# Performance work log

Measured on AMD Instinct MI355X. Metric: run time of the kernel, lower is better.

The kernel has to match this reference:

```python
import jax, jax.numpy as jnp
import numpy as np

N, E, D, G, NTYPES = 50000, 400000, 64, 512, 64


def _bn(x, g, b):
    # BatchNorm1d in training mode: biased batch stats, eps=1e-5, affine g/b
    mu = x.mean(0)
    var = ((x - mu) ** 2).mean(0)
    return g * (x - mu) * jax.lax.rsqrt(var + 1e-5) + b


def _rotmat(a):
    t, p, q = a[0], a[1], a[2]
    ct, st = jnp.cos(t), jnp.sin(t)
    cp, sp = jnp.cos(p), jnp.sin(p)
    cq, sq = jnp.cos(q), jnp.sin(q)
    z = jnp.zeros(())
    o = jnp.ones(())
    Rt = jnp.array([[ct, -st, z], [st, ct, z], [z, z, o]])
    Rp = jnp.array([[cp, z, -sp], [z, o, z], [sp, z, cp]])
    Rq = jnp.array([[o, z, z], [z, cq, -sq], [z, sq, cq]])
    return Rt @ Rp @ Rq


def _egat(src, dst, nf, ef, Wnode, bnode, Wni, Wnj, Wfij, attn, H):
    # DGL EGATConv: edge feats from src/dst node + edge projections, edge-softmax attention over dst
    n = nf.shape[0]
    f_out = jax.nn.leaky_relu((nf @ Wni)[src] + (nf @ Wnj)[dst] + ef @ Wfij)  # [E, H*D]
    f_out = f_out.reshape(-1, H, D)
    e = (f_out * attn[None]).sum(-1)  # [E, H]
    emax = jax.ops.segment_max(e, dst, num_segments=n)
    ee = jnp.exp(e - emax[dst])
    a = ee / jax.ops.segment_sum(ee, dst, num_segments=n)[dst]
    hsrc = (nf @ Wnode + bnode).reshape(n, H, D)[src]
    h_out = jax.ops.segment_sum(hsrc * a[:, :, None], dst, num_segments=n)  # [N, H, D]
    return h_out, f_out


def _layer(src, dst, nh, eh, p, H, last):
    Wnode, bnode, Wni, Wnj, Wfij, attn, bnn_g, bnn_b, bne_g, bne_b, Wpn, bpn, Wpe, bpe = p
    hn, he = _egat(src, dst, nh, eh, Wnode, bnode, Wni, Wnj, Wfij, attn, H)
    if last:
        hn, he = hn.mean(1), he.mean(1)
    else:
        hn, he = hn.reshape(hn.shape[0], -1), he.reshape(he.shape[0], -1)
    hn = _bn(hn, bnn_g, bnn_b)
    he = _bn(he, bne_g, bne_b)
    return hn @ Wpn + bpn + nh, he @ Wpe + bpe + eh


def setup_inputs():
    key = jax.random.key(0)
    kit = iter(jax.random.split(key, 64))

    def rn(shape, s=0.05):
        return jax.random.normal(next(kit), shape, dtype=jnp.float32) * s

    inp = {}
    inp["ntype"] = jax.random.randint(next(kit), (N, 1), 0, NTYPES)
    inp["src"] = jax.random.randint(next(kit), (E,), 0, N)
    inp["dst"] = jax.random.randint(next(kit), (E,), 0, N)
    inp["graph_ids"] = jnp.sort(jax.random.randint(next(kit), (N,), 0, G))
    inp["angles_rot"] = rn((3,), 1.0)
    inp["angles_ref"] = rn((3,), 1.0)
    inp["efeats"] = rn((E, 3), 1.0)
    inp["emb_table"] = rn((NTYPES, D))
    inp["enc_W"] = rn((D, D)); inp["enc_b"] = jnp.zeros((D,))
    inp["ee_W1"] = rn((3, D)); inp["ee_b1"] = jnp.zeros((D,))
    inp["ee_W2"] = rn((D, D)); inp["ee_b2"] = jnp.zeros((D,))
    for nm in ["enc_bn1", "enc_bn2", "ee_bn1", "ee_bn2"]:
        inp[nm + "_g"] = jnp.ones((D,)); inp[nm + "_b"] = jnp.zeros((D,))
    for l, H in [(0, 2), (1, 1)]:
        p = "l%d_" % l
        inp[p + "Wnode"] = rn((D, H * D)); inp[p + "bnode"] = jnp.zeros((H * D,))
        inp[p + "Wni"] = rn((D, H * D)); inp[p + "Wnj"] = rn((D, H * D)); inp[p + "Wfij"] = rn((D, H * D))
        inp[p + "attn"] = rn((H, D))
        inp[p + "bnn_g"] = jnp.ones((H * D,)); inp[p + "bnn_b"] = jnp.zeros((H * D,))
        inp[p + "bne_g"] = jnp.ones((H * D,)); inp[p + "bne_b"] = jnp.zeros((H * D,))
        inp[p + "Wpn"] = rn((H * D, D)); inp[p + "bpn"] = jnp.zeros((D,))
        inp[p + "Wpe"] = rn((H * D, D)); inp[p + "bpe"] = jnp.zeros((D,))
    inp["dec_W"] = rn((4, D, D)); inp["dec_b"] = jnp.zeros((4, D))
    inp["dec_bn_g"] = jnp.ones((4, D)); inp["dec_bn_b"] = jnp.zeros((4, D))
    inp["dec_prelu"] = jnp.full((4,), 0.25, dtype=jnp.float32)
    inp["dec_Wout"] = rn((D, 1)); inp["dec_bout"] = jnp.zeros((1,))
    return inp


def reference(efeats, emb_table, enc_bn1_g, enc_bn1_b, enc_W, enc_b, enc_bn2_g, enc_bn2_b, ee_W1, ee_b1, ee_bn1_g, ee_bn1_b, ee_W2, ee_b2, ee_bn2_g, ee_bn2_b, l0_Wnode, l0_bnode, l0_Wni, l0_Wnj, l0_Wfij, l0_attn, l0_bnn_g, l0_bnn_b, l0_bne_g, l0_bne_b, l0_Wpn, l0_bpn, l0_Wpe, l0_bpe, l1_Wnode, l1_bnode, l1_Wni, l1_Wnj, l1_Wfij, l1_attn, l1_bnn_g, l1_bnn_b, l1_bne_g, l1_bne_b, l1_Wpn, l1_bpn, l1_Wpe, l1_bpe, dec_W, dec_b, dec_bn_g, dec_bn_b, dec_prelu, dec_Wout, dec_bout, ntype, src, dst, graph_ids, angles_rot, angles_ref):
    # node encoder: Embedding -> BN -> ReLU -> Linear -> BN -> ReLU
    nh = emb_table[ntype[:, 0]]
    nh = jax.nn.relu(_bn(nh, enc_bn1_g, enc_bn1_b))
    nh = jax.nn.relu(_bn(nh @ enc_W + enc_b, enc_bn2_g, enc_bn2_b))

    def edge_enc(f):
        h = jax.nn.relu(_bn(f @ ee_W1 + ee_b1, ee_bn1_g, ee_bn1_b))
        return jax.nn.relu(_bn(h @ ee_W2 + ee_b2, ee_bn2_g, ee_bn2_b))

    # rotation matrices built from sampled angles; torch.tensor([...]) detaches -> stop_gradient
    R_rot = jax.lax.stop_gradient(_rotmat(angles_rot))
    R_ref = -jax.lax.stop_gradient(_rotmat(angles_ref))
    eh = edge_enc(efeats @ R_rot) + edge_enc(efeats @ R_ref)

    p0 = (l0_Wnode, l0_bnode, l0_Wni, l0_Wnj, l0_Wfij, l0_attn, l0_bnn_g, l0_bnn_b, l0_bne_g, l0_bne_b, l0_Wpn, l0_bpn, l0_Wpe, l0_bpe)
    p1 = (l1_Wnode, l1_bnode, l1_Wni, l1_Wnj, l1_Wfij, l1_attn, l1_bnn_g, l1_bnn_b, l1_bne_g, l1_bne_b, l1_Wpn, l1_bpn, l1_Wpe, l1_bpe)
    nh, eh = _layer(src, dst, nh, eh, p0, 2, False)
    h1 = nh
    nh, eh = _layer(src, dst, nh, eh, p1, 1, True)
    h2 = nh

    h = nh
    for i in range(4):
        h = _bn(h @ dec_W[i] + dec_b[i], dec_bn_g[i], dec_bn_b[i])
        h = jnp.where(h >= 0.0, h, dec_prelu[i] * h)
    h = h @ dec_Wout + dec_bout
    # dgl.sum_nodes: per-graph sum over batched graphs
    return (h1, h2, jax.ops.segment_sum(h, graph_ids, num_segments=G))
```

## Files before the change

### kernel.cpp

```cpp
#include <hip/hip_runtime.h>
#include <math.h>

#define NN 50000
#define NE 400000
#define NG 512
#define EPS 1e-5f
#define NSLOT 256

typedef unsigned int u32;
typedef unsigned short u16;

typedef __attribute__((ext_vector_type(8))) short s16x8;
typedef __attribute__((ext_vector_type(4))) float f32x4;

__device__ __forceinline__ float b2f(u16 h) { return __uint_as_float(((u32)h) << 16); }
__device__ __forceinline__ u16 f2b(float f) {
    u32 x = __float_as_uint(f);
    u32 r = x + 0x7fffu + ((x >> 16) & 1u);
    return (u16)(r >> 16);
}
struct alignas(16) U16x8 { u16 s[8]; };
struct alignas(8) U16x4 { u16 s[4]; };
struct alignas(4) U16x2 { u16 s[2]; };

__device__ __forceinline__ void f4add(float4& a, const float4 b) {
    a.x += b.x; a.y += b.y; a.z += b.z; a.w += b.w;
}

__global__ void setup_kernel(const float* __restrict__ ang_rot, const float* __restrict__ ang_ref,
                             const float* __restrict__ W1, float* __restrict__ RWrot,
                             float* __restrict__ RWref) {
    int c = threadIdx.x;
    for (int which = 0; which < 2; ++which) {
        const float* a = which ? ang_ref : ang_rot;
        float t = a[0], p = a[1], q = a[2];
        float ct = cosf(t), st = sinf(t);
        float cp = cosf(p), sp = sinf(p);
        float cq = cosf(q), sq = sinf(q);
        float Rt[3][3] = {{ct, -st, 0.f}, {st, ct, 0.f}, {0.f, 0.f, 1.f}};
        float Rp[3][3] = {{cp, 0.f, -sp}, {0.f, 1.f, 0.f}, {sp, 0.f, cp}};
        float Rq[3][3] = {{1.f, 0.f, 0.f}, {0.f, cq, -sq}, {0.f, sq, cq}};
        float Rtp[3][3], R[3][3];
        for (int i = 0; i < 3; ++i)
            for (int j = 0; j < 3; ++j) {
                float s = 0.f;
                for (int k = 0; k < 3; ++k) s += Rt[i][k] * Rp[k][j];
                Rtp[i][j] = s;
            }
        for (int i = 0; i < 3; ++i)
            for (int j = 0; j < 3; ++j) {
                float s = 0.f;
                for (int k = 0; k < 3; ++k) s += Rtp[i][k] * Rq[k][j];
                R[i][j] = s;
            }
        float sgn = which ? -1.f : 1.f;
        float* RW = which ? RWref : RWrot;
        if (c < 64) {
            for (int j = 0; j < 3; ++j) {
                float s = 0.f;
                for (int m = 0; m < 3; ++m) s += sgn * R[j][m] * W1[m * 64 + c];
                RW[j * 64 + c] = s;
            }
        }
    }
}

#define NWT 17
struct WtJobs {
    const float* W[NWT];
    u16* WT[NWT];
    int K[NWT];
    int C[NWT];
};
__global__ __launch_bounds__(256) void wt_all_kernel(WtJobs jobs) {
    int job = blockIdx.x >> 5;
    int idx = ((blockIdx.x & 31) << 8) + threadIdx.x;
    int K = jobs.K[job], C = jobs.C[job];
    if (idx >= K * C) return;
    int k = idx / C, c = idx - k * C;
    jobs.WT[job][c * K + k] = f2b(jobs.W[job][idx]);
}

__global__ __launch_bounds__(256) void hist_kernel(const int* __restrict__ dst, int E,
                                                   int* __restrict__ deg) {
    int e = blockIdx.x * 256 + threadIdx.x;
    if (e < E) atomicAdd(&deg[dst[e]], 1);
}

__global__ __launch_bounds__(256) void scan_part_kernel(const int* __restrict__ deg,
                                                        int* __restrict__ bsum, int n) {
    int i = blockIdx.x * 256 + threadIdx.x;
    int v = (i < n) ? deg[i] : 0;
#pragma unroll
    for (int off = 1; off < 64; off <<= 1) v += __shfl_xor(v, off, 64);
    __shared__ int ws[4];
    if ((threadIdx.x & 63) == 0) ws[threadIdx.x >> 6] = v;
    __syncthreads();
    if (threadIdx.x == 0) bsum[blockIdx.x] = ws[0] + ws[1] + ws[2] + ws[3];
}

__global__ __launch_bounds__(256) void scan_top_kernel(int* __restrict__ bsum, int nb,
                                                       int* __restrict__ rowptr, int n,
                                                       int total) {
    __shared__ int s[256];
    int tid = threadIdx.x;
    s[tid] = (tid < nb) ? bsum[tid] : 0;
    __syncthreads();
    for (int off = 1; off < 256; off <<= 1) {
        int v = (tid >= off) ? s[tid - off] : 0;
        __syncthreads();
        s[tid] += v;
        __syncthreads();
    }
    if (tid < nb) bsum[tid] = (tid == 0) ? 0 : s[tid - 1];
    if (tid == 0) rowptr[n] = total;
}

__global__ __launch_bounds__(256) void scan_fill_kernel(const int* __restrict__ deg,
                                                        const int* __restrict__ bsum,
                                                        int* __restrict__ rowptr,
                                                        int* __restrict__ curs, int n) {
    __shared__ int s[256];
    int tid = threadIdx.x;
    int i = blockIdx.x * 256 + tid;
    int v = (i < n) ? deg[i] : 0;
    s[tid] = v;
    __syncthreads();
    for (int off = 1; off < 256; off <<= 1) {
        int t = (tid >= off) ? s[tid - off] : 0;
        __syncthreads();
        s[tid] += t;
        __syncthreads();
    }
    if (i < n) {
        int excl = s[tid] - v + bsum[blockIdx.x];
        rowptr[i] = excl;
        curs[i] = excl;
    }
}

__global__ __launch_bounds__(256) void fill_kernel(const int* __restrict__ src,
                                                   const int* __restrict__ dst, int E,
                                                   int* __restrict__ curs,
                                                   int* __restrict__ epos,
                                                   int* __restrict__ esrc) {
    int e = blockIdx.x * 256 + threadIdx.x;
    if (e >= E) return;
    int pos = atomicAdd(&curs[dst[e]], 1);
    epos[e] = pos;
    esrc[pos] = src[e];
}

__global__ __launch_bounds__(256) void gather_emb_kernel(const int* __restrict__ ntype,
                                                         const float* __restrict__ emb,
                                                         u16* __restrict__ out, int n) {
    long i = (long)blockIdx.x * 256 + threadIdx.x;
    long e = i >> 3;
    if (e >= n) return;
    int c0 = (int)(i & 7) * 8;
    int t = ntype[e];
    float4 a = *(const float4*)&emb[(long)t * 64 + c0];
    float4 b = *(const float4*)&emb[(long)t * 64 + c0 + 4];
    U16x8 o;
    o.s[0] = f2b(a.x); o.s[1] = f2b(a.y); o.s[2] = f2b(a.z); o.s[3] = f2b(a.w);
    o.s[4] = f2b(b.x); o.s[5] = f2b(b.y); o.s[6] = f2b(b.z); o.s[7] = f2b(b.w);
    *(U16x8*)&out[e * 64 + c0] = o;
}

__global__ __launch_bounds__(256) void efstats_kernel(const float* __restrict__ ef, int E,
                                                      float* __restrict__ raw) {
    int tid = threadIdx.x;
    float a[9];
#pragma unroll
    for (int j = 0; j < 9; ++j) a[j] = 0.f;
    for (long e = (long)blockIdx.x * 256 + tid; e < E; e += (long)gridDim.x * 256) {
        float f0 = ef[e * 3 + 0], f1 = ef[e * 3 + 1], f2 = ef[e * 3 + 2];
        a[0] += f0; a[1] += f1; a[2] += f2;
        a[3] += f0 * f0; a[4] += f1 * f1; a[5] += f2 * f2;
        a[6] += f0 * f1; a[7] += f0 * f2; a[8] += f1 * f2;
    }
#pragma unroll
    for (int off = 1; off < 64; off <<= 1)
#pragma unroll
        for (int j = 0; j < 9; ++j) a[j] += __shfl_xor(a[j], off, 64);
    __shared__ float sred[4][9];
    int wv = tid >> 6, ln = tid & 63;
    if (ln == 0)
#pragma unroll
        for (int j = 0; j < 9; ++j) sred[wv][j] = a[j];
    __syncthreads();
    if (tid < 9) {
        float v = sred[0][tid] + sred[1][tid] + sred[2][tid] + sred[3][tid];
        atomicAdd(&raw[(size_t)(blockIdx.x & (NSLOT - 1)) * 16 + tid], v);
    }
}

__global__ void ee_stats_kernel(const float* __restrict__ efraw, const float* __restrict__ RWrot,
                                const float* __restrict__ RWref, const float* __restrict__ b1,
                                float* __restrict__ S_rot, float* __restrict__ S_ref, int E) {
    __shared__ float m[9];
    int t = threadIdx.x;
    if (t < 9) {
        float s = 0.f;
        for (int r = 0; r < NSLOT; ++r) s += efraw[r * 16 + t];
        m[t] = s;
    }
    __syncthreads();
    int br = t >> 6, c = t & 63;
    const float* RW = br ? RWref : RWrot;
    float* S = br ? S_ref : S_rot;
    float w0 = RW[c], w1 = RW[64 + c], w2 = RW[128 + c];
    float bb = b1[c];
    float mw = m[0] * w0 + m[1] * w1 + m[2] * w2;
    float sum = mw + (float)E * bb;
    float quad = m[3] * w0 * w0 + m[4] * w1 * w1 + m[5] * w2 * w2 +
                 2.f * (m[6] * w0 * w1 + m[7] * w0 * w2 + m[8] * w1 * w2);
    float ss = quad + 2.f * bb * mw + (float)E * bb * bb;
    S[c] = sum;
    S[64 + c] = ss;
}

template <int COLS>
__global__ __launch_bounds__(256) void colstats_kernel(const u16* __restrict__ xv, int rows,
                                                       float* __restrict__ raw) {
    constexpr int TPR = COLS / 8;
    constexpr int RPB = 256 / TPR;
    __shared__ float4 sA[256], sB[256], sC[256], sD[256];
    int tid = threadIdx.x;
    int c8 = tid % TPR;
    int rl = tid / TPR;
    float s[8], q[8];
#pragma unroll
    for (int j = 0; j < 8; ++j) { s[j] = 0.f; q[j] = 0.f; }
    const long stride = (long)gridDim.x * RPB;
    for (long r = (long)blockIdx.x * RPB + rl; r < rows; r += stride) {
        U16x8 t = *(const U16x8*)&xv[r * COLS + c8 * 8];
#pragma unroll
        for (int j = 0; j < 8; ++j) {
            float v = b2f(t.s[j]);
            s[j] += v;
            q[j] += v * v;
        }
    }
    sA[tid] = make_float4(s[0], s[1], s[2], s[3]);
    sB[tid] = make_float4(s[4], s[5], s[6], s[7]);
    sC[tid] = make_float4(q[0], q[1], q[2], q[3]);
    sD[tid] = make_float4(q[4], q[5], q[6], q[7]);
    __syncthreads();
    for (int off = 128; off >= TPR; off >>= 1) {
        if (tid < off) {
            f4add(sA[tid], sA[tid + off]); f4add(sB[tid], sB[tid + off]);
            f4add(sC[tid], sC[tid + off]); f4add(sD[tid], sD[tid + off]);
        }
        __syncthreads();
    }
    if (tid < TPR) {
        float* slot = raw + (size_t)(blockIdx.x & (NSLOT - 1)) * 256;
        int c = tid * 8;
        float4 a = sA[tid], b = sB[tid], cq = sC[tid], d = sD[tid];
        atomicAdd(&slot[c + 0], a.x); atomicAdd(&slot[c + 1], a.y);
        atomicAdd(&slot[c + 2], a.z); atomicAdd(&slot[c + 3], a.w);
        atomicAdd(&slot[c + 4], b.x); atomicAdd(&slot[c + 5], b.y);
        atomicAdd(&slot[c + 6], b.z); atomicAdd(&slot[c + 7], b.w);
        atomicAdd(&slot[COLS + c + 0], cq.x); atomicAdd(&slot[COLS + c + 1], cq.y);
        atomicAdd(&slot[COLS + c + 2], cq.z); atomicAdd(&slot[COLS + c + 3], cq.w);
        atomicAdd(&slot[COLS + c + 4], d.x); atomicAdd(&slot[COLS + c + 5], d.y);
        atomicAdd(&slot[COLS + c + 6], d.z); atomicAdd(&slot[COLS + c + 7], d.w);
    }
}

__global__ __launch_bounds__(256) void finalize_stats_kernel(const float* __restrict__ raw,
                                                             float* __restrict__ stats, int n) {
    int i = threadIdx.x;
    if (i >= n) return;
    float s = 0.f;
    for (int r = 0; r < NSLOT; ++r) s += raw[r * 256 + i];
    stats[i] = s;
}

__global__ __launch_bounds__(256) void bn_act_kernel(const u16* __restrict__ x,
                                                     u16* __restrict__ y, long rows, int cols,
                                                     const float* __restrict__ acc,
                                                     const float* __restrict__ g,
                                                     const float* __restrict__ b,
                                                     float inv_rows) {
    long i = (long)blockIdx.x * 256 + threadIdx.x;
    long total8 = rows * (long)cols / 8;
    if (i >= total8) return;
    long base = i * 8;
    int c0 = (int)(base % cols);
    U16x8 xv = *(const U16x8*)&x[base];
    U16x8 o;
#pragma unroll
    for (int j = 0; j < 8; ++j) {
        int c = c0 + j;
        float mu = acc[c] * inv_rows;
        float var = acc[cols + c] * inv_rows - mu * mu;
        float al = g[c] * rsqrtf(fmaxf(var, 0.f) + EPS);
        float be = b[c] - mu * al;
        o.s[j] = f2b(fmaxf(al * b2f(xv.s[j]) + be, 0.f));
    }
    *(U16x8*)&y[base] = o;
}
// ... 109 lines not shown
                float vv = acc[r] + bb;
                if (resv) {
                    if (RBF) vv += b2f(((const u16*)resv)[orr * COLS + col]);
                    else vv += ((const float*)resv)[orr * COLS + col];
                }
                if (OBF) ((u16*)Yv)[orr * COLS + col] = f2b(vv);
                else ((float*)Yv)[orr * COLS + col] = vv;
                if (SOUT) { fs += vv; fq += vv * vv; }
            }
            if (SOUT) {
                fs += __shfl_xor(fs, 16, 64); fs += __shfl_xor(fs, 32, 64);
                fq += __shfl_xor(fq, 16, 64); fq += __shfl_xor(fq, 32, 64);
                if (q == 0) {
                    atomicAdd(&ssum[col], fs);
                    atomicAdd(&ssq[col], fq);
                }
            }
        }
    }
    if (SOUT) {
        __syncthreads();
        float* slot = raw + (size_t)(blockIdx.x & (NSLOT - 1)) * 256;
        for (int i = tid; i < COLS; i += 256) {
            atomicAdd(&slot[i], ssum[i]);
            atomicAdd(&slot[COLS + i], ssq[i]);
        }
    }
}

template <int COLS, bool XBF>
__global__ __launch_bounds__(256) void mfma_mm3_kernel(
    const void* __restrict__ Xv, const u16* __restrict__ WT0, const u16* __restrict__ WT1,
    const u16* __restrict__ WT2, const float* __restrict__ bias2, u16* __restrict__ Y0,
    u16* __restrict__ Y1, u16* __restrict__ Y2, int rows) {
    constexpr int NCT = COLS / 16;
    const int tid = threadIdx.x;
    const int lane = tid & 63, wv = tid >> 6;
    const int q = lane >> 4, rr = lane & 15;
    const long r0 = ((long)blockIdx.x * 4 + wv) * 16;
    if (r0 >= rows) return;
    s16x8 afr[2];
#pragma unroll
    for (int kk = 0; kk < 2; ++kk) {
        if (XBF) {
            afr[kk] = *(const s16x8*)((const u16*)Xv + (r0 + rr) * 64 + kk * 32 + q * 8);
        } else {
            const float* xp = (const float*)Xv + (r0 + rr) * 64 + kk * 32 + q * 8;
            float4 t0 = *(const float4*)xp;
            float4 t1 = *(const float4*)(xp + 4);
            union { u16 u[8]; s16x8 s; } o;
            o.u[0] = f2b(t0.x); o.u[1] = f2b(t0.y); o.u[2] = f2b(t0.z); o.u[3] = f2b(t0.w);
            o.u[4] = f2b(t1.x); o.u[5] = f2b(t1.y); o.u[6] = f2b(t1.z); o.u[7] = f2b(t1.w);
            afr[kk] = o.s;
        }
    }
    const u16* wts[3] = {WT0, WT1, WT2};
    u16* ys[3] = {Y0, Y1, Y2};
#pragma unroll
    for (int m = 0; m < 3; ++m) {
#pragma unroll
        for (int ct = 0; ct < NCT; ++ct) {
            f32x4 acc = (f32x4){0.f, 0.f, 0.f, 0.f};
#pragma unroll
            for (int kk = 0; kk < 2; ++kk) {
                s16x8 bfr = *(const s16x8*)&wts[m][(size_t)(ct * 16 + rr) * 64 + kk * 32 + q * 8];
                acc = __builtin_amdgcn_mfma_f32_16x16x32_bf16(afr[kk], bfr, acc, 0, 0, 0);
            }
            int col = ct * 16 + rr;
            float bb = (m == 2) ? bias2[col] : 0.f;
#pragma unroll
            for (int r = 0; r < 4; ++r) {
                long orr = r0 + q * 4 + r;
                ys[m][orr * COLS + col] = f2b(acc[r] + bb);
            }
        }
    }
}

__global__ __launch_bounds__(256) void mfma_ee_kernel(
    const float* __restrict__ ef, const float* __restrict__ RW, const float* __restrict__ b1v,
    const u16* __restrict__ W2T, const float* __restrict__ b2, u16* __restrict__ T2, int E,
    const float* __restrict__ stats, const float* __restrict__ g, const float* __restrict__ b,
    float inv_rows, float* __restrict__ raw) {
    __shared__ float rws[192];
    __shared__ float al[64], be[64];
    __shared__ float ssum[64], ssq[64];
    const int tid = threadIdx.x;
    if (tid < 192) rws[tid] = RW[tid];
    if (tid < 64) {
        float mu = stats[tid] * inv_rows;
        float var = stats[64 + tid] * inv_rows - mu * mu;
        float a = g[tid] * rsqrtf(fmaxf(var, 0.f) + EPS);
        al[tid] = a;
        be[tid] = b[tid] - mu * a + a * b1v[tid];
        ssum[tid] = 0.f;
        ssq[tid] = 0.f;
    }
    __syncthreads();
    const int lane = tid & 63, wv = tid >> 6;
    const int q = lane >> 4, rr = lane & 15;
    const long r0 = ((long)blockIdx.x * 4 + wv) * 16;
    const long ar = r0 + rr;
    float e0 = ef[ar * 3], e1 = ef[ar * 3 + 1], e2 = ef[ar * 3 + 2];
    s16x8 afr[2];
#pragma unroll
    for (int kk = 0; kk < 2; ++kk) {
        union { u16 u[8]; s16x8 v; } t;
#pragma unroll
        for (int j = 0; j < 8; ++j) {
            int k = kk * 32 + q * 8 + j;
            float tv = e0 * rws[k] + e1 * rws[64 + k] + e2 * rws[128 + k];
            t.u[j] = f2b(fmaxf(al[k] * tv + be[k], 0.f));
        }
        afr[kk] = t.v;
    }
    f32x4 acc[4];
#pragma unroll
    for (int ct = 0; ct < 4; ++ct) {
        acc[ct] = (f32x4){0.f, 0.f, 0.f, 0.f};
#pragma unroll
        for (int kk = 0; kk < 2; ++kk) {
            s16x8 bfr = *(const s16x8*)&W2T[(size_t)(ct * 16 + rr) * 64 + kk * 32 + q * 8];
            acc[ct] = __builtin_amdgcn_mfma_f32_16x16x32_bf16(afr[kk], bfr, acc[ct], 0, 0, 0);
        }
    }
#pragma unroll
    for (int ct = 0; ct < 4; ++ct) {
        int col = ct * 16 + rr;
        float bb = b2[col];
        float s = 0.f, qq = 0.f;
#pragma unroll
        for (int r = 0; r < 4; ++r) {
            long orr = r0 + q * 4 + r;
            float v = acc[ct][r] + bb;
            T2[orr * 64 + col] = f2b(v);
            s += v;
            qq += v * v;
        }
        s += __shfl_xor(s, 16, 64); s += __shfl_xor(s, 32, 64);
        qq += __shfl_xor(qq, 16, 64); qq += __shfl_xor(qq, 32, 64);
        if (q == 0) {
            atomicAdd(&ssum[col], s);
            atomicAdd(&ssq[col], qq);
        }
    }
    __syncthreads();
    if (tid < 64) {
        float* slot = raw + (size_t)(blockIdx.x & (NSLOT - 1)) * 256;
        atomicAdd(&slot[tid], ssum[tid]);
        atomicAdd(&slot[64 + tid], ssq[tid]);
    }
}

template <int COLS, bool WRITE_F, bool SOUT>
__global__ __launch_bounds__(256) void mfma_egat_kernel(
    const u16* __restrict__ EH, const u16* __restrict__ WT, const u16* __restrict__ NI,
    const u16* __restrict__ NJ, const int* __restrict__ src, const int* __restrict__ dst,
    const int* __restrict__ epos, const float* __restrict__ attn, u16* __restrict__ Fout,
    float* __restrict__ eatt, int E, float* __restrict__ raw) {
    constexpr int H = COLS / 64;
    constexpr int NCT = COLS / 16;
    constexpr int FSTR = COLS + 8;
    __shared__ float ssum[SOUT ? COLS : 1];
    __shared__ float ssq[SOUT ? COLS : 1];
    __shared__ u16 fts[WRITE_F ? 64 * FSTR : 1];
    const int tid = threadIdx.x;
    if (SOUT) {
        for (int i = tid; i < COLS; i += 256) { ssum[i] = 0.f; ssq[i] = 0.f; }
        __syncthreads();
    }
    const int lane = tid & 63, wv = tid >> 6;
    const int q = lane >> 4, rr = lane & 15;
    const long r0 = ((long)blockIdx.x * 4 + wv) * 16;
    s16x8 afr[2];
#pragma unroll
    for (int kk = 0; kk < 2; ++kk)
        afr[kk] = *(const s16x8*)&EH[(r0 + rr) * 64 + kk * 32 + q * 8];
    int sidx[4], didx[4];
#pragma unroll
    for (int r = 0; r < 4; ++r) {
        long orr = r0 + q * 4 + r;
        sidx[r] = src[orr];
        didx[r] = dst[orr];
    }
    f32x4 acc[NCT];
#pragma unroll
    for (int ct = 0; ct < NCT; ++ct) {
        acc[ct] = (f32x4){0.f, 0.f, 0.f, 0.f};
#pragma unroll
        for (int kk = 0; kk < 2; ++kk) {
            s16x8 bfr = *(const s16x8*)&WT[(size_t)(ct * 16 + rr) * 64 + kk * 32 + q * 8];
            acc[ct] = __builtin_amdgcn_mfma_f32_16x16x32_bf16(afr[kk], bfr, acc[ct], 0, 0, 0);
        }
    }
    float part[H][4];
#pragma unroll
    for (int h = 0; h < H; ++h)
#pragma unroll
        for (int r = 0; r < 4; ++r) part[h][r] = 0.f;
#pragma unroll
    for (int ct = 0; ct < NCT; ++ct) {
        int col = ct * 16 + rr;
        float av = attn[col];
        const int h = (H == 2) ? (ct >> 2) : 0;
        float fs = 0.f, fq = 0.f;
#pragma unroll
        for (int r = 0; r < 4; ++r) {
            float f = acc[ct][r] + b2f(NI[(size_t)sidx[r] * COLS + col]) +
                      b2f(NJ[(size_t)didx[r] * COLS + col]);
            f = (f >= 0.f) ? f : 0.01f * f;
            if (WRITE_F) fts[(wv * 16 + q * 4 + r) * FSTR + col] = f2b(f);
            part[h][r] += f * av;
            if (SOUT) { fs += f; fq += f * f; }
        }
        if (SOUT) {
            fs += __shfl_xor(fs, 16, 64); fs += __shfl_xor(fs, 32, 64);
            fq += __shfl_xor(fq, 16, 64); fq += __shfl_xor(fq, 32, 64);
            if (q == 0) {
                atomicAdd(&ssum[col], fs);
                atomicAdd(&ssq[col], fq);
            }
        }
    }
#pragma unroll
    for (int h = 0; h < H; ++h)
#pragma unroll
        for (int r = 0; r < 4; ++r) {
            float p = part[h][r];
            p += __shfl_xor(p, 1, 64);
            p += __shfl_xor(p, 2, 64);
            p += __shfl_xor(p, 4, 64);
            p += __shfl_xor(p, 8, 64);
            part[h][r] = p;
        }
    if (rr == 0) {
#pragma unroll
        for (int r = 0; r < 4; ++r) {
            long pos = epos[r0 + q * 4 + r];
            if (H == 2) {
                eatt[pos * 2 + 0] = part[0][r];
                eatt[pos * 2 + 1] = part[1][r];
            } else {
                eatt[pos] = part[0][r];
            }
        }
    }
    if (WRITE_F) {
        __syncthreads();
        const long rb = (long)blockIdx.x * 64;
        constexpr int CH = COLS / 8;
        for (int i = tid; i < 64 * CH; i += 256) {
            int row = i / CH, c8 = i % CH;
            U16x8 v = *(const U16x8*)&fts[row * FSTR + c8 * 8];
            *(U16x8*)&Fout[(rb + row) * COLS + c8 * 8] = v;
        }
    }
    if (SOUT) {
        __syncthreads();
        float* slot = raw + (size_t)(blockIdx.x & (NSLOT - 1)) * 256;
        for (int i = tid; i < COLS; i += 256) {
            atomicAdd(&slot[i], ssum[i]);
            atomicAdd(&slot[COLS + i], ssq[i]);
        }
    }
}

__global__ __launch_bounds__(256) void mfma_pe_kernel(
    const u16* __restrict__ X, const u16* __restrict__ WT, const float* __restrict__ bias,
    u16* __restrict__ EHio, int E, const float* __restrict__ stats, const float* __restrict__ g,
    const float* __restrict__ b, float inv_rows) {
    __shared__ float al[128], be[128];
    const int tid = threadIdx.x;
    if (tid < 128) {
        float mu = stats[tid] * inv_rows;
        float var = stats[128 + tid] * inv_rows - mu * mu;
        float a = g[tid] * rsqrtf(fmaxf(var, 0.f) + EPS);
        al[tid] = a;
        be[tid] = b[tid] - mu * a;
    }
    __syncthreads();
    const int lane = tid & 63, wv = tid >> 6;
    const int q = lane >> 4, rr = lane & 15;
    const long r0 = ((long)blockIdx.x * 4 + wv) * 16;
    s16x8 afr[4];
#pragma unroll
    for (int kk = 0; kk < 4; ++kk) {
        U16x8 t = *(const U16x8*)&X[(r0 + rr) * 128 + kk * 32 + q * 8];
        union { u16 u[8]; s16x8 v; } o;
#pragma unroll
        for (int j = 0; j < 8; ++j) {
            int k = kk * 32 + q * 8 + j;
            o.u[j] = f2b(al[k] * b2f(t.s[j]) + be[k]);
        }
        afr[kk] = o.v;
    }
    f32x4 acc[4];
#pragma unroll
    for (int ct = 0; ct < 4; ++ct) {
        acc[ct] = (f32x4){0.f, 0.f, 0.f, 0.f};
#pragma unroll
        for (int kk = 0; kk < 4; ++kk) {
            s16x8 bfr = *(const s16x8*)&WT[(size_t)(ct * 16 + rr) * 128 + kk * 32 + q * 8];
            acc[ct] = __builtin_amdgcn_mfma_f32_16x16x32_bf16(afr[kk], bfr, acc[ct], 0, 0, 0);
        }
    }
#pragma unroll
    for (int ct = 0; ct < 4; ++ct) {
        int col = ct * 16 + rr;
        float bb = bias[col];
#pragma unroll
        for (int r = 0; r < 4; ++r) {
            long orr = r0 + q * 4 + r;
            float v = acc[ct][r] + bb + b2f(EHio[orr * 64 + col]);
            EHio[orr * 64 + col] = f2b(v);
        }
    }
}

template <int COLS, bool SOUT>
__global__ __launch_bounds__(256) void csr_aggregate_kernel(
    const int* __restrict__ rowptr, const int* __restrict__ esrc,
    const float* __restrict__ eatt, const u16* __restrict__ nodeh, float* __restrict__ hout,
    int n, float* __restrict__ raw) {
    constexpr int H = COLS / 64;
    constexpr int TPN = COLS / 2;
    constexpr int NPB = 256 / TPN;
    __shared__ float ssum[SOUT ? COLS : 1];
    __shared__ float ssq[SOUT ? COLS : 1];
    int tid = threadIdx.x;
    if (SOUT) {
        for (int i = tid; i < COLS; i += 256) { ssum[i] = 0.f; ssq[i] = 0.f; }
        __syncthreads();
    }
    int node = blockIdx.x * NPB + tid / TPN;
    bool act = node < n;
    int c = (tid % TPN) * 2;
    float a0 = 0.f, a1 = 0.f;
    if (act) {
        int h = (H == 2) ? (c >> 6) : 0;
        int p0 = rowptr[node], p1 = rowptr[node + 1];
        float m = -INFINITY, s = 0.f;
        for (int p = p0; p < p1; ++p) {
            float v = eatt[(long)p * H + h];
            float mn = fmaxf(m, v);
            s = s * expf(m - mn) + expf(v - mn);
            m = mn;
        }
        float inv = (s > 0.f) ? 1.f / s : 0.f;
        for (int p = p0; p < p1; ++p) {
            float w = expf(eatt[(long)p * H + h] - m) * inv;
            U16x2 v = *(const U16x2*)&nodeh[(long)esrc[p] * COLS + c];
            a0 += b2f(v.s[0]) * w;
            a1 += b2f(v.s[1]) * w;
        }
        *(float2*)&hout[(long)node * COLS + c] = make_float2(a0, a1);
    }
    if (SOUT) {
        if (act) {
            atomicAdd(&ssum[c], a0);
            atomicAdd(&ssum[c + 1], a1);
            atomicAdd(&ssq[c], a0 * a0);
            atomicAdd(&ssq[c + 1], a1 * a1);
        }
        __syncthreads();
        float* slot = raw + (size_t)(blockIdx.x & (NSLOT - 1)) * 256;
        for (int i = tid; i < COLS; i += 256) {
            atomicAdd(&slot[i], ssum[i]);
            atomicAdd(&slot[COLS + i], ssq[i]);
        }
    }
}

__global__ __launch_bounds__(256) void decoder_out_kernel(
    const u16* __restrict__ t3, const float* __restrict__ stats, const float* __restrict__ g,
    const float* __restrict__ b, const float* __restrict__ prelu, const float* __restrict__ Wout,
    const float* __restrict__ bout, const int* __restrict__ gid, float* __restrict__ pool,
    int rows, float inv_rows) {
    int tid = threadIdx.x;
    long r = (long)blockIdx.x * 4 + (tid >> 6);
    if (r >= rows) return;
    int k = tid & 63;
    float mu = stats[k] * inv_rows;
    float var = stats[64 + k] * inv_rows - mu * mu;
    float al = g[k] * rsqrtf(fmaxf(var, 0.f) + EPS);
    float be = b[k] - mu * al;
    float a = prelu[3];
    float v = al * b2f(t3[r * 64 + k]) + be;
    v = (v >= 0.f) ? v : a * v;
    v *= Wout[k];
#pragma unroll
    for (int off = 1; off < 64; off <<= 1) v += __shfl_xor(v, off, 64);
    if (k == 0) atomicAdd(&pool[gid[r]], v + bout[0]);
}

extern "C" void kernel_launch(void* const* d_in, const int* in_sizes, int n_in, void* d_out,
                              int out_size, void* d_ws, size_t ws_size, hipStream_t stream) {
    if (n_in < 57) return;
    const int* ntype = (const int*)d_in[0];
    const int* src = (const int*)d_in[1];
    const int* dst = (const int*)d_in[2];
    const int* gid = (const int*)d_in[3];
    const float* ang_rot = (const float*)d_in[4];
    const float* ang_ref = (const float*)d_in[5];
    const float* efeats = (const float*)d_in[6];
    const float* emb = (const float*)d_in[7];
    const float* enc_W = (const float*)d_in[8];
    const float* enc_b = (const float*)d_in[9];
    const float* ee_W1 = (const float*)d_in[10];
    const float* ee_b1 = (const float*)d_in[11];
    const float* ee_W2 = (const float*)d_in[12];
    const float* ee_b2 = (const float*)d_in[13];
    const float* enc_bn1_g = (const float*)d_in[14];
    const float* enc_bn1_b = (const float*)d_in[15];
    const float* enc_bn2_g = (const float*)d_in[16];
    const float* enc_bn2_b = (const float*)d_in[17];
    const float* ee_bn1_g = (const float*)d_in[18];
    const float* ee_bn1_b = (const float*)d_in[19];
    const float* ee_bn2_g = (const float*)d_in[20];
    const float* ee_bn2_b = (const float*)d_in[21];
    const float* l0_Wnode = (const float*)d_in[22];
    const float* l0_bnode = (const float*)d_in[23];
    const float* l0_Wni = (const float*)d_in[24];
    const float* l0_Wnj = (const float*)d_in[25];
    const float* l0_Wfij = (const float*)d_in[26];
    const float* l0_attn = (const float*)d_in[27];
    const float* l0_bnn_g = (const float*)d_in[28];
    const float* l0_bnn_b = (const float*)d_in[29];
    const float* l0_bne_g = (const float*)d_in[30];
    const float* l0_bne_b = (const float*)d_in[31];
    const float* l0_Wpn = (const float*)d_in[32];
    const float* l0_bpn = (const float*)d_in[33];
    const float* l0_Wpe = (const float*)d_in[34];
    const float* l0_bpe = (const float*)d_in[35];
    const float* l1_Wnode = (const float*)d_in[36];
    const float* l1_bnode = (const float*)d_in[37];
    const float* l1_Wni = (const float*)d_in[38];
    const float* l1_Wnj = (const float*)d_in[39];
    const float* l1_Wfij = (const float*)d_in[40];
    const float* l1_attn = (const float*)d_in[41];
    const float* l1_bnn_g = (const float*)d_in[42];
    const float* l1_bnn_b = (const float*)d_in[43];
    const float* l1_Wpn = (const float*)d_in[46];
    const float* l1_bpn = (const float*)d_in[47];
    const float* dec_W = (const float*)d_in[50];
    const float* dec_b = (const float*)d_in[51];
    const float* dec_bn_g = (const float*)d_in[52];
    const float* dec_bn_b = (const float*)d_in[53];
    const float* dec_prelu = (const float*)d_in[54];
    const float* dec_Wout = (const float*)d_in[55];
    const float* dec_bout = (const float*)d_in[56];

    float* out = (float*)d_out;
    float* H1 = out;
    float* H2 = out + (long)NN * 64;
    float* POOL = out + (long)NN * 128;

    char* base = (char*)d_ws;
    size_t off = 0;
    auto alloc = [&](size_t bytes) -> void* {
        off = (off + 255) & ~(size_t)255;
        void* p = base + off;
        off += bytes;
        return p;
    };
    u16* EH = (u16*)alloc((size_t)NE * 64 * 2);
    u16* F128 = (u16*)alloc((size_t)NE * 128 * 2);
    float* EATT = (float*)alloc((size_t)NE * 2 * 4);
    u16* NX = (u16*)alloc((size_t)NN * 64 * 2);
    u16* NI = (u16*)alloc((size_t)NN * 128 * 2);
    u16* NJ = (u16*)alloc((size_t)NN * 128 * 2);
    u16* NHH = (u16*)alloc((size_t)NN * 128 * 2);
    float* HOUT0 = (float*)alloc((size_t)NN * 128 * 4);
    float* HOUT1 = (float*)alloc((size_t)NN * 64 * 4);
    int* ROWPTR = (int*)alloc((size_t)(NN + 1) * 4);
    int* CURS = (int*)alloc((size_t)NN * 4);
    int* EPOS = (int*)alloc((size_t)NE * 4);
    int* ESRC = (int*)alloc((size_t)NE * 4);
    int* BSUM = (int*)alloc((size_t)256 * 4);
    float* RWrot = (float*)alloc(256 * 4);
    float* RWref = (float*)alloc(256 * 4);
    u16* EncWT = (u16*)alloc(4096 * 2);
    u16* W2T = (u16*)alloc(4096 * 2);
    u16* Wni0T = (u16*)alloc(8192 * 2);
    u16* Wnj0T = (u16*)alloc(8192 * 2);
    u16* Wnd0T = (u16*)alloc(8192 * 2);
    u16* WfijT0 = (u16*)alloc(8192 * 2);
    u16* Wpn0T = (u16*)alloc(8192 * 2);
    u16* WpeT = (u16*)alloc(8192 * 2);
    u16* Wni1T = (u16*)alloc(4096 * 2);
    u16* Wnj1T = (u16*)alloc(4096 * 2);
    u16* Wnd1T = (u16*)alloc(4096 * 2);
    u16* WfijT1 = (u16*)alloc(4096 * 2);
    u16* Wpn1T = (u16*)alloc(4096 * 2);
    u16* DecT0 = (u16*)alloc(4096 * 2);
    u16* DecT1 = (u16*)alloc(4096 * 2);
    u16* DecT2 = (u16*)alloc(4096 * 2);
    u16* DecT3 = (u16*)alloc(4096 * 2);
    float* STATS = (float*)alloc((size_t)13 * 256 * 4);
    char* zstart = base + ((off + 255) & ~(size_t)255);
    int* DEG = (int*)alloc((size_t)NN * 4);
    float* STATS_RAW = (float*)alloc((size_t)13 * NSLOT * 256 * 4);
    float* RAWEF = (float*)alloc((size_t)NSLOT * 16 * 4);
    char* zend = base + off;
    if (ws_size < off) return;

    u16* T2a = F128;
    u16* T2b = F128 + (size_t)NE * 64;
    u16* NX0 = F128;
    u16* NT = F128 + (size_t)NE * 64;
    u16* DT0 = NI;
    u16* DT1 = NJ;

    auto RAW = [&](int idx) { return STATS_RAW + (size_t)idx * NSLOT * 256; };
    float* S_enc1 = STATS + 0 * 256;
    float* S_enc2 = STATS + 1 * 256;
    float* S_ee2r = STATS + 3 * 256;
    float* S_ee1r = STATS + 2 * 256;
    float* S_ee1f = STATS + 4 * 256;
    float* S_ee2f = STATS + 5 * 256;
    float* S_bnn0 = STATS + 6 * 256;
    float* S_bne0 = STATS + 7 * 256;
    float* S_bnn1 = STATS + 8 * 256;
    float* S_d0 = STATS + 9 * 256;
    float* S_d1 = STATS + 10 * 256;
    float* S_d2 = STATS + 11 * 256;
    float* S_d3 = STATS + 12 * 256;

    const float invN = 1.f / (float)NN;
    const float invE = 1.f / (float)NE;
    const int GS = 640;
    const int MFB = NE / 64;
    const int NNB = (NN + 63) / 64;
    const int NB = (NN + 255) / 256;

    hipMemsetAsync(zstart, 0, (size_t)(zend - zstart), stream);
    hipMemsetAsync(POOL, 0, (size_t)NG * 4, stream);

    setup_kernel<<<1, 64, 0, stream>>>(ang_rot, ang_ref, ee_W1, RWrot, RWref);
    {
        WtJobs j;
        const float* Ws[NWT] = {enc_W,  ee_W2,  l0_Wni, l0_Wnj, l0_Wnode, l0_Wfij,
                                l0_Wpn, l0_Wpe, l1_Wni, l1_Wnj, l1_Wnode, l1_Wfij,
                                l1_Wpn, dec_W,  dec_W + 4096, dec_W + 8192, dec_W + 12288};
        u16* Ts[NWT] = {EncWT, W2T, Wni0T, Wnj0T, Wnd0T, WfijT0, Wpn0T, WpeT, Wni1T,
                        Wnj1T, Wnd1T, WfijT1, Wpn1T, DecT0, DecT1, DecT2, DecT3};
        int Ks[NWT] = {64, 64, 64, 64, 64, 64, 128, 128, 64, 64, 64, 64, 64, 64, 64, 64, 64};
        int Cs[NWT] = {64, 64, 128, 128, 128, 128, 64, 64, 64, 64, 64, 64, 64, 64, 64, 64, 64};
        for (int i = 0; i < NWT; ++i) { j.W[i] = Ws[i]; j.WT[i] = Ts[i]; j.K[i] = Ks[i]; j.C[i] = Cs[i]; }
        wt_all_kernel<<<NWT * 32, 256, 0, stream>>>(j);
    }

    hist_kernel<<<(NE + 255) / 256, 256, 0, stream>>>(dst, NE, DEG);
    scan_part_kernel<<<NB, 256, 0, stream>>>(DEG, BSUM, NN);
    scan_top_kernel<<<1, 256, 0, stream>>>(BSUM, NB, ROWPTR, NN, NE);
    scan_fill_kernel<<<NB, 256, 0, stream>>>(DEG, BSUM, ROWPTR, CURS, NN);
    fill_kernel<<<(NE + 255) / 256, 256, 0, stream>>>(src, dst, NE, CURS, EPOS, ESRC);

    gather_emb_kernel<<<(NN * 8 + 255) / 256, 256, 0, stream>>>(ntype, emb, NX0, NN);
    colstats_kernel<64><<<GS, 256, 0, stream>>>(NX0, NN, RAW(0));
    finalize_stats_kernel<<<1, 256, 0, stream>>>(RAW(0), S_enc1, 128);
    mfma_mm_kernel<64, 64, true, false, true, true><<<NNB, 256, 0, stream>>>(
        NX0, EncWT, enc_b, nullptr, NT, NN, 2, S_enc1, enc_bn1_g, enc_bn1_b, invN, nullptr, 0,
        RAW(1));
    finalize_stats_kernel<<<1, 256, 0, stream>>>(RAW(1), S_enc2, 128);
    bn_act_kernel<<<(NN * 8 + 255) / 256, 256, 0, stream>>>(NT, NX, NN, 64, S_enc2, enc_bn2_g,
                                                            enc_bn2_b, invN);

    efstats_kernel<<<256, 256, 0, stream>>>(efeats, NE, RAWEF);
    ee_stats_kernel<<<1, 128, 0, stream>>>(RAWEF, RWrot, RWref, ee_b1, S_ee1r, S_ee1f, NE);
    mfma_ee_kernel<<<MFB, 256, 0, stream>>>(efeats, RWrot, ee_b1, W2T, ee_b2, T2a, NE, S_ee1r,
                                            ee_bn1_g, ee_bn1_b, invE, RAW(3));
    mfma_ee_kernel<<<MFB, 256, 0, stream>>>(efeats, RWref, ee_b1, W2T, ee_b2, T2b, NE, S_ee1f,
                                            ee_bn1_g, ee_bn1_b, invE, RAW(5));
    finalize_stats_kernel<<<1, 256, 0, stream>>>(RAW(3), S_ee2r, 128);
    finalize_stats_kernel<<<1, 256, 0, stream>>>(RAW(5), S_ee2f, 128);
    ee_merge_kernel<<<(int)(((long)NE * 8 + 255) / 256), 256, 0, stream>>>(
        T2a, T2b, EH, S_ee2r, S_ee2f, ee_bn2_g, ee_bn2_b, invE);

    mfma_mm3_kernel<128, true><<<NNB, 256, 0, stream>>>(NX, Wni0T, Wnj0T, Wnd0T, l0_bnode, NI,
                                                        NJ, NHH, NN);
    mfma_egat_kernel<128, true, true><<<MFB, 256, 0, stream>>>(
        EH, WfijT0, NI, NJ, src, dst, EPOS, l0_attn, F128, EATT, NE, RAW(7));
    finalize_stats_kernel<<<1, 256, 0, stream>>>(RAW(7), S_bne0, 256);
    csr_aggregate_kernel<128, true><<<(NN + 3) / 4, 256, 0, stream>>>(ROWPTR, ESRC, EATT, NHH,
                                                                      HOUT0, NN, RAW(6));
    finalize_stats_kernel<<<1, 256, 0, stream>>>(RAW(6), S_bnn0, 256);
    mfma_mm_kernel<128, 64, false, true, false, false><<<NNB, 256, 0, stream>>>(
        HOUT0, Wpn0T, l0_bpn, NX, H1, NN, 1, S_bnn0, l0_bnn_g, l0_bnn_b, invN, nullptr, 0,
        nullptr);
    mfma_pe_kernel<<<MFB, 256, 0, stream>>>(F128, WpeT, l0_bpe, EH, NE, S_bne0, l0_bne_g,
                                            l0_bne_b, invE);

    mfma_mm3_kernel<64, false><<<NNB, 256, 0, stream>>>(H1, Wni1T, Wnj1T, Wnd1T, l1_bnode, NI,
                                                        NJ, NHH, NN);
    mfma_egat_kernel<64, false, false><<<MFB, 256, 0, stream>>>(
        EH, WfijT1, NI, NJ, src, dst, EPOS, l1_attn, nullptr, EATT, NE, nullptr);
    csr_aggregate_kernel<64, true><<<(NN + 7) / 8, 256, 0, stream>>>(ROWPTR, ESRC, EATT, NHH,
                                                                     HOUT1, NN, RAW(8));
    finalize_stats_kernel<<<1, 256, 0, stream>>>(RAW(8), S_bnn1, 128);
    mfma_mm_kernel<64, 64, false, false, false, false><<<NNB, 256, 0, stream>>>(
        HOUT1, Wpn1T, l1_bpn, H1, H2, NN, 1, S_bnn1, l1_bnn_g, l1_bnn_b, invN, nullptr, 0,
        nullptr);

    mfma_mm_kernel<64, 64, false, false, true, true><<<NNB, 256, 0, stream>>>(
        H2, DecT0, dec_b, nullptr, DT0, NN, 0, nullptr, nullptr, nullptr, 0.f, nullptr, 0,
        RAW(9));
    finalize_stats_kernel<<<1, 256, 0, stream>>>(RAW(9), S_d0, 128);
    mfma_mm_kernel<64, 64, true, false, true, true><<<NNB, 256, 0, stream>>>(
        DT0, DecT1, dec_b + 64, nullptr, DT1, NN, 3, S_d0, dec_bn_g, dec_bn_b, invN, dec_prelu,
        0, RAW(10));
    finalize_stats_kernel<<<1, 256, 0, stream>>>(RAW(10), S_d1, 128);
    mfma_mm_kernel<64, 64, true, false, true, true><<<NNB, 256, 0, stream>>>(
        DT1, DecT2, dec_b + 128, nullptr, DT0, NN, 3, S_d1, dec_bn_g + 64, dec_bn_b + 64, invN,
        dec_prelu, 1, RAW(11));
    finalize_stats_kernel<<<1, 256, 0, stream>>>(RAW(11), S_d2, 128);
    mfma_mm_kernel<64, 64, true, false, true, true><<<NNB, 256, 0, stream>>>(
        DT0, DecT3, dec_b + 192, nullptr, DT1, NN, 3, S_d2, dec_bn_g + 128, dec_bn_b + 128,
        invN, dec_prelu, 2, RAW(12));
    finalize_stats_kernel<<<1, 256, 0, stream>>>(RAW(12), S_d3, 128);
    decoder_out_kernel<<<(NN + 3) / 4, 256, 0, stream>>>(DT1, S_d3, dec_bn_g + 192,
                                                         dec_bn_b + 192, dec_prelu, dec_Wout,
                                                         dec_bout, gid, POOL, NN, invN);
}
```

Before: 864.2 us.

## Sort edges by destination and recompute layer-0 edge features instead of storing them

The fill kernel now permutes edges into destination-sorted (CSR) order. It writes src, dst and the raw edge features in that order, so every later edge kernel works in sorted order and the epos scatter indirection goes away. The layer-0 EGAT kernel no longer writes the 128-wide edge feature tensor F. A new fused kernel recomputes F (the Wfij MFMA plus NI/NJ gathers and leaky ReLU), applies the batch norm, and runs the Wpe projection from shared memory. This trades a large global write and re-read for a second pass of gathers and MFMAs. Destination-sorted order should also make the NJ gathers more cache-friendly.

```diff
diff --git a/kernel.cpp b/kernel.cpp
--- a/kernel.cpp
+++ b/kernel.cpp
@@ -140,15 +140,21 @@
 }
 
 __global__ __launch_bounds__(256) void fill_kernel(const int* __restrict__ src,
-                                                   const int* __restrict__ dst, int E,
+                                                   const int* __restrict__ dst,
+                                                   const float* __restrict__ ef, int E,
                                                    int* __restrict__ curs,
-                                                   int* __restrict__ epos,
-                                                   int* __restrict__ esrc) {
+                                                   int* __restrict__ esrc,
+                                                   int* __restrict__ dsts,
+                                                   float* __restrict__ efp) {
     int e = blockIdx.x * 256 + threadIdx.x;
     if (e >= E) return;
-    int pos = atomicAdd(&curs[dst[e]], 1);
-    epos[e] = pos;
+    int d = dst[e];
+    int pos = atomicAdd(&curs[d], 1);
     esrc[pos] = src[e];
+    dsts[pos] = d;
+    efp[(long)pos * 3 + 0] = ef[(long)e * 3 + 0];
+    efp[(long)pos * 3 + 1] = ef[(long)e * 3 + 1];
+    efp[(long)pos * 3 + 2] = ef[(long)e * 3 + 2];
 }
 
 __global__ __launch_bounds__(256) void gather_emb_kernel(const int* __restrict__ ntype,
@@ -564,18 +570,15 @@
     }
 }
 
-template <int COLS, bool WRITE_F, bool SOUT>
+template <int COLS, bool SOUT>
 __global__ __launch_bounds__(256) void mfma_egat_kernel(
     const u16* __restrict__ EH, const u16* __restrict__ WT, const u16* __restrict__ NI,
-    const u16* __restrict__ NJ, const int* __restrict__ src, const int* __restrict__ dst,
-    const int* __restrict__ epos, const float* __restrict__ attn, u16* __restrict__ Fout,
-    float* __restrict__ eatt, int E, float* __restrict__ raw) {
+    const u16* __restrict__ NJ, const int* __restrict__ srcs, const int* __restrict__ dsts,
+    const float* __restrict__ attn, float* __restrict__ eatt, int E, float* __restrict__ raw) {
     constexpr int H = COLS / 64;
     constexpr int NCT = COLS / 16;
-    constexpr int FSTR = COLS + 8;
     __shared__ float ssum[SOUT ? COLS : 1];
     __shared__ float ssq[SOUT ? COLS : 1];
-    __shared__ u16 fts[WRITE_F ? 64 * FSTR : 1];
     const int tid = threadIdx.x;
     if (SOUT) {
         for (int i = tid; i < COLS; i += 256) { ssum[i] = 0.f; ssq[i] = 0.f; }
@@ -592,8 +595,8 @@
 #pragma unroll
     for (int r = 0; r < 4; ++r) {
         long orr = r0 + q * 4 + r;
-        sidx[r] = src[orr];
-        didx[r] = dst[orr];
+        sidx[r] = srcs[orr];
+        didx[r] = dsts[orr];
     }
     f32x4 acc[NCT];
 #pragma unroll
@@ -621,7 +624,6 @@
             float f = acc[ct][r] + b2f(NI[(size_t)sidx[r] * COLS + col]) +
                       b2f(NJ[(size_t)didx[r] * COLS + col]);
             f = (f >= 0.f) ? f : 0.01f * f;
-            if (WRITE_F) fts[(wv * 16 + q * 4 + r) * FSTR + col] = f2b(f);
             part[h][r] += f * av;
             if (SOUT) { fs += f; fq += f * f; }
         }
@@ -648,23 +650,13 @@
     if (rr == 0) {
 #pragma unroll
         for (int r = 0; r < 4; ++r) {
-            long pos = epos[r0 + q * 4 + r];
+            long pos = r0 + q * 4 + r;
             if (H == 2) {
                 eatt[pos * 2 + 0] = part[0][r];
                 eatt[pos * 2 + 1] = part[1][r];
             } else {
                 eatt[pos] = part[0][r];
             }
-        }
-    }
-    if (WRITE_F) {
-        __syncthreads();
-        const long rb = (long)blockIdx.x * 64;
-        constexpr int CH = COLS / 8;
-        for (int i = tid; i < 64 * CH; i += 256) {
-            int row = i / CH, c8 = i % CH;
-            U16x8 v = *(const U16x8*)&fts[row * FSTR + c8 * 8];
-            *(U16x8*)&Fout[(rb + row) * COLS + c8 * 8] = v;
         }
     }
     if (SOUT) {
@@ -677,11 +669,15 @@
     }
 }
 
-__global__ __launch_bounds__(256) void mfma_pe_kernel(
-    const u16* __restrict__ X, const u16* __restrict__ WT, const float* __restrict__ bias,
-    u16* __restrict__ EHio, int E, const float* __restrict__ stats, const float* __restrict__ g,
-    const float* __restrict__ b, float inv_rows) {
+__global__ __launch_bounds__(256) void mfma_pe2_kernel(
+    const u16* __restrict__ EH, const u16* __restrict__ WfijT, const u16* __restrict__ WpeT,
+    const u16* __restrict__ NI, const u16* __restrict__ NJ, const int* __restrict__ srcs,
+    const int* __restrict__ dsts, const float* __restrict__ bias, u16* __restrict__ EHio, int E,
+    const float* __restrict__ stats, const float* __restrict__ g, const float* __restrict__ b,
+    float inv_rows) {
+    constexpr int FSTR = 136;
     __shared__ float al[128], be[128];
+    __shared__ u16 fts[64 * FSTR];
     const int tid = threadIdx.x;
     if (tid < 128) {
         float mu = stats[tid] * inv_rows;
@@ -694,36 +690,53 @@
     const int lane = tid & 63, wv = tid >> 6;
     const int q = lane >> 4, rr = lane & 15;
     const long r0 = ((long)blockIdx.x * 4 + wv) * 16;
-    s16x8 afr[4];
-#pragma unroll
-    for (int kk = 0; kk < 4; ++kk) {
-        U16x8 t = *(const U16x8*)&X[(r0 + rr) * 128 + kk * 32 + q * 8];
-        union { u16 u[8]; s16x8 v; } o;
-#pragma unroll
-        for (int j = 0; j < 8; ++j) {
-            int k = kk * 32 + q * 8 + j;
-            o.u[j] = f2b(al[k] * b2f(t.s[j]) + be[k]);
-        }
-        afr[kk] = o.v;
-    }
-    f32x4 acc[4];
+    s16x8 afr[2];
+#pragma unroll
+    for (int kk = 0; kk < 2; ++kk)
+        afr[kk] = *(const s16x8*)&EH[(r0 + rr) * 64 + kk * 32 + q * 8];
+    int sidx[4], didx[4];
+#pragma unroll
+    for (int r = 0; r < 4; ++r) {
+        long orr = r0 + q * 4 + r;
+        sidx[r] = srcs[orr];
+        didx[r] = dsts[orr];
+    }
+#pragma unroll
+    for (int ct = 0; ct < 8; ++ct) {
+        f32x4 acc = (f32x4){0.f, 0.f, 0.f, 0.f};
+#pragma unroll
+        for (int kk = 0; kk < 2; ++kk) {
+            s16x8 bfr = *(const s16x8*)&WfijT[(size_t)(ct * 16 + rr) * 64 + kk * 32 + q * 8];
+            acc = __builtin_amdgcn_mfma_f32_16x16x32_bf16(afr[kk], bfr, acc, 0, 0, 0);
+        }
+        int col = ct * 16 + rr;
+#pragma unroll
+        for (int r = 0; r < 4; ++r) {
+            float f = acc[r] + b2f(NI[(size_t)sidx[r] * 128 + col]) +
+                      b2f(NJ[(size_t)didx[r] * 128 + col]);
+            f = (f >= 0.f) ? f : 0.01f * f;
+            fts[(wv * 16 + q * 4 + r) * FSTR + col] = f2b(al[col] * f + be[col]);
+        }
+    }
+    __syncthreads();
+    s16x8 afr2[4];
+#pragma unroll
+    for (int kk = 0; kk < 4; ++kk)
+        afr2[kk] = *(const s16x8*)&fts[(wv * 16 + rr) * FSTR + kk * 32 + q * 8];
 #pragma unroll
     for (int ct = 0; ct < 4; ++ct) {
-        acc[ct] = (f32x4){0.f, 0.f, 0.f, 0.f};
+        f32x4 acc = (f32x4){0.f, 0.f, 0.f, 0.f};
 #pragma unroll
         for (int kk = 0; kk < 4; ++kk) {
-            s16x8 bfr = *(const s16x8*)&WT[(size_t)(ct * 16 + rr) * 128 + kk * 32 + q * 8];
-            acc[ct] = __builtin_amdgcn_mfma_f32_16x16x32_bf16(afr[kk], bfr, acc[ct], 0, 0, 0);
-        }
-    }
-#pragma unroll
-    for (int ct = 0; ct < 4; ++ct) {
+            s16x8 bfr = *(const s16x8*)&WpeT[(size_t)(ct * 16 + rr) * 128 + kk * 32 + q * 8];
+            acc = __builtin_amdgcn_mfma_f32_16x16x32_bf16(afr2[kk], bfr, acc, 0, 0, 0);
+        }
         int col = ct * 16 + rr;
         float bb = bias[col];
 #pragma unroll
         for (int r = 0; r < 4; ++r) {
             long orr = r0 + q * 4 + r;
-            float v = acc[ct][r] + bb + b2f(EHio[orr * 64 + col]);
+            float v = acc[r] + bb + b2f(EHio[orr * 64 + col]);
             EHio[orr * 64 + col] = f2b(v);
         }
     }
@@ -876,7 +889,7 @@
         return p;
     };
     u16* EH = (u16*)alloc((size_t)NE * 64 * 2);
-    u16* F128 = (u16*)alloc((size_t)NE * 128 * 2);
+    u16* T2AB = (u16*)alloc((size_t)NE * 128 * 2);
     float* EATT = (float*)alloc((size_t)NE * 2 * 4);
     u16* NX = (u16*)alloc((size_t)NN * 64 * 2);
     u16* NI = (u16*)alloc((size_t)NN * 128 * 2);
@@ -886,8 +899,9 @@
     float* HOUT1 = (float*)alloc((size_t)NN * 64 * 4);
     int* ROWPTR = (int*)alloc((size_t)(NN + 1) * 4);
     int* CURS = (int*)alloc((size_t)NN * 4);
-    int* EPOS = (int*)alloc((size_t)NE * 4);
     int* ESRC = (int*)alloc((size_t)NE * 4);
+    int* DSTS = (int*)alloc((size_t)NE * 4);
+    float* EFP = (float*)alloc((size_t)NE * 3 * 4);
     int* BSUM = (int*)alloc((size_t)256 * 4);
     float* RWrot = (float*)alloc(256 * 4);
     float* RWref = (float*)alloc(256 * 4);
@@ -916,18 +930,18 @@
     char* zend = base + off;
     if (ws_size < off) return;
 
-    u16* T2a = F128;
-    u16* T2b = F128 + (size_t)NE * 64;
-    u16* NX0 = F128;
-    u16* NT = F128 + (size_t)NE * 64;
+    u16* T2a = T2AB;
+    u16* T2b = T2AB + (size_t)NE * 64;
+    u16* NX0 = T2AB;
+    u16* NT = T2AB + (size_t)NE * 64;
     u16* DT0 = NI;
     u16* DT1 = NJ;
 
     auto RAW = [&](int idx) { return STATS_RAW + (size_t)idx * NSLOT * 256; };
     float* S_enc1 = STATS + 0 * 256;
     float* S_enc2 = STATS + 1 * 256;
+    float* S_ee1r = STATS + 2 * 256;
     float* S_ee2r = STATS + 3 * 256;
-    float* S_ee1r = STATS + 2 * 256;
     float* S_ee1f = STATS + 4 * 256;
     float* S_ee2f = STATS + 5 * 256;
     float* S_bnn0 = STATS + 6 * 256;
@@ -966,7 +980,8 @@
     scan_part_kernel<<<NB, 256, 0, stream>>>(DEG, BSUM, NN);
     scan_top_kernel<<<1, 256, 0, stream>>>(BSUM, NB, ROWPTR, NN, NE);
     scan_fill_kernel<<<NB, 256, 0, stream>>>(DEG, BSUM, ROWPTR, CURS, NN);
-    fill_kernel<<<(NE + 255) / 256, 256, 0, stream>>>(src, dst, NE, CURS, EPOS, ESRC);
+    fill_kernel<<<(NE + 255) / 256, 256, 0, stream>>>(src, dst, efeats, NE, CURS, ESRC, DSTS,
+                                                      EFP);
 
     gather_emb_kernel<<<(NN * 8 + 255) / 256, 256, 0, stream>>>(ntype, emb, NX0, NN);
     colstats_kernel<64><<<GS, 256, 0, stream>>>(NX0, NN, RAW(0));
@@ -980,9 +995,9 @@
 
     efstats_kernel<<<256, 256, 0, stream>>>(efeats, NE, RAWEF);
     ee_stats_kernel<<<1, 128, 0, stream>>>(RAWEF, RWrot, RWref, ee_b1, S_ee1r, S_ee1f, NE);
-    mfma_ee_kernel<<<MFB, 256, 0, stream>>>(efeats, RWrot, ee_b1, W2T, ee_b2, T2a, NE, S_ee1r,
+    mfma_ee_kernel<<<MFB, 256, 0, stream>>>(EFP, RWrot, ee_b1, W2T, ee_b2, T2a, NE, S_ee1r,
                                             ee_bn1_g, ee_bn1_b, invE, RAW(3));
-    mfma_ee_kernel<<<MFB, 256, 0, stream>>>(efeats, RWref, ee_b1, W2T, ee_b2, T2b, NE, S_ee1f,
+    mfma_ee_kernel<<<MFB, 256, 0, stream>>>(EFP, RWref, ee_b1, W2T, ee_b2, T2b, NE, S_ee1f,
                                             ee_bn1_g, ee_bn1_b, invE, RAW(5));
     finalize_stats_kernel<<<1, 256, 0, stream>>>(RAW(3), S_ee2r, 128);
     finalize_stats_kernel<<<1, 256, 0, stream>>>(RAW(5), S_ee2f, 128);
@@ -991,8 +1006,8 @@
 
     mfma_mm3_kernel<128, true><<<NNB, 256, 0, stream>>>(NX, Wni0T, Wnj0T, Wnd0T, l0_bnode, NI,
                                                         NJ, NHH, NN);
-    mfma_egat_kernel<128, true, true><<<MFB, 256, 0, stream>>>(
-        EH, WfijT0, NI, NJ, src, dst, EPOS, l0_attn, F128, EATT, NE, RAW(7));
+    mfma_egat_kernel<128, true><<<MFB, 256, 0, stream>>>(EH, WfijT0, NI, NJ, ESRC, DSTS, l0_attn,
+                                                         EATT, NE, RAW(7));
     finalize_stats_kernel<<<1, 256, 0, stream>>>(RAW(7), S_bne0, 256);
     csr_aggregate_kernel<128, true><<<(NN + 3) / 4, 256, 0, stream>>>(ROWPTR, ESRC, EATT, NHH,
                                                                       HOUT0, NN, RAW(6));
@@ -1000,13 +1015,13 @@
     mfma_mm_kernel<128, 64, false, true, false, false><<<NNB, 256, 0, stream>>>(
         HOUT0, Wpn0T, l0_bpn, NX, H1, NN, 1, S_bnn0, l0_bnn_g, l0_bnn_b, invN, nullptr, 0,
         nullptr);
-    mfma_pe_kernel<<<MFB, 256, 0, stream>>>(F128, WpeT, l0_bpe, EH, NE, S_bne0, l0_bne_g,
-                                            l0_bne_b, invE);
+    mfma_pe2_kernel<<<MFB, 256, 0, stream>>>(EH, WfijT0, WpeT, NI, NJ, ESRC, DSTS, l0_bpe, EH,
+                                             NE, S_bne0, l0_bne_g, l0_bne_b, invE);
 
     mfma_mm3_kernel<64, false><<<NNB, 256, 0, stream>>>(H1, Wni1T, Wnj1T, Wnd1T, l1_bnode, NI,
                                                         NJ, NHH, NN);
-    mfma_egat_kernel<64, false, false><<<MFB, 256, 0, stream>>>(
-        EH, WfijT1, NI, NJ, src, dst, EPOS, l1_attn, nullptr, EATT, NE, nullptr);
+    mfma_egat_kernel<64, false><<<MFB, 256, 0, stream>>>(EH, WfijT1, NI, NJ, ESRC, DSTS, l1_attn,
+                                                         EATT, NE, nullptr);
     csr_aggregate_kernel<64, true><<<(NN + 7) / 8, 256, 0, stream>>>(ROWPTR, ESRC, EATT, NHH,
                                                                      HOUT1, NN, RAW(8));
     finalize_stats_kernel<<<1, 256, 0, stream>>>(RAW(8), S_bnn1, 128);
```

Result: slower. 919.5 us (+6.4%).
